# Optimization experiments

Measured on AMD Instinct MI355X. Metric: run time of the kernel, lower is better.

Reference implementation:

```python
import jax, jax.numpy as jnp
import numpy as np

B, T, N_IN, N = 64, 512, 256, 512

def setup_inputs() -> dict:
    key = jax.random.key(0)
    k1, k2, k3 = jax.random.split(key, 3)
    x = jax.random.normal(k1, (B, T, N_IN), dtype=jnp.float32)
    # match nn.Linear default init scale roughly (uniform +-1/sqrt(fan_in))
    W_ih = jax.random.uniform(k2, (N, N_IN), dtype=jnp.float32, minval=-1.0, maxval=1.0) / np.sqrt(N_IN)
    W_hh = jax.random.uniform(k3, (N, N), dtype=jnp.float32, minval=-1.0, maxval=1.0) / np.sqrt(N)
    return {"x": x, "W_ih": W_ih, "W_hh": W_hh}

def reference(x, W_ih, W_hh):
    # h_t = W_hh @ tanh(h_{t-1}) + W_ih @ x_t, h_0 = 0 (pre-activation hidden stored)
    # x: [B, T, n_in] (batch_first). Precompute input projections for all steps.
    xp = jnp.einsum('btc,nc->tbn', x, W_ih)  # [T, B, N]

    def step(h, xp_t):
        h_new = jnp.tanh(h) @ W_hh.T + xp_t  # [B, N]
        return h_new, h_new

    h0 = jnp.zeros((x.shape[0], W_hh.shape[0]), dtype=x.dtype)
    _, hs = jax.lax.scan(step, h0, xp)  # hs: [T, B, N]
    return jnp.swapaxes(hs, 0, 1)  # [B, T, N], batch_first output
```

## Files before the change

kernel.cpp:

```cpp
#include <hip/hip_runtime.h>
#include <hip/hip_bf16.h>
#include <stdint.h>

#define B_   64
#define T_   512
#define NIN_ 256
#define N_   512

typedef _Float16 half2_t __attribute__((ext_vector_type(2)));

#if defined(__has_builtin)
#if __has_builtin(__builtin_amdgcn_fdot2)
#define HAVE_FDOT2 1
#endif
#endif

__device__ __forceinline__ float dot2acc(unsigned int a, unsigned int b, float c) {
#ifdef HAVE_FDOT2
  return __builtin_amdgcn_fdot2(__builtin_bit_cast(half2_t, a),
                                __builtin_bit_cast(half2_t, b), c, false);
#else
  half2_t ha = __builtin_bit_cast(half2_t, a), hb = __builtin_bit_cast(half2_t, b);
  c += (float)ha[0] * (float)hb[0];
  c += (float)ha[1] * (float)hb[1];
  return c;
#endif
}

__device__ __forceinline__ float fast_tanh(float x) {
  float e = __expf(2.0f * x);
  return 1.0f - 2.0f / (e + 1.0f);
}

__global__ __launch_bounds__(256) void xproj(const float* __restrict__ x,
                                             const float* __restrict__ Wih,
                                             float* __restrict__ out) {
  const int tid = threadIdx.x;
  const int bm = blockIdx.x;
  const int bn = blockIdx.y;
  const int tm = tid & 15;
  const int tn = tid >> 4;
  const int m0 = bm << 7;
  const int n0 = bn << 7;

  __shared__ float xt[32][132];
  __shared__ float wt[32][132];

  float acc[8][8];
#pragma unroll
  for (int i = 0; i < 8; ++i) {
#pragma unroll
    for (int j = 0; j < 8; ++j) acc[i][j] = 0.f;
  }

  for (int ko = 0; ko < NIN_; ko += 32) {
#pragma unroll
    for (int it = 0; it < 4; ++it) {
      const int fidx = it * 256 + tid;
      const int mm = fidx >> 3;
      const int k4 = (fidx & 7) << 2;
      const float4 vx = *(const float4*)(x + (size_t)(m0 + mm) * NIN_ + ko + k4);
      xt[k4 + 0][mm] = vx.x; xt[k4 + 1][mm] = vx.y;
      xt[k4 + 2][mm] = vx.z; xt[k4 + 3][mm] = vx.w;
      const float4 vw = *(const float4*)(Wih + (size_t)(n0 + mm) * NIN_ + ko + k4);
      wt[k4 + 0][mm] = vw.x; wt[k4 + 1][mm] = vw.y;
      wt[k4 + 2][mm] = vw.z; wt[k4 + 3][mm] = vw.w;
    }
    __syncthreads();
#pragma unroll 4
    for (int kk = 0; kk < 32; ++kk) {
      float a[8], b[8];
      *(float4*)&a[0] = *(const float4*)&xt[kk][8 * tm];
      *(float4*)&a[4] = *(const float4*)&xt[kk][8 * tm + 4];
      *(float4*)&b[0] = *(const float4*)&wt[kk][8 * tn];
      *(float4*)&b[4] = *(const float4*)&wt[kk][8 * tn + 4];
#pragma unroll
      for (int i = 0; i < 8; ++i) {
#pragma unroll
        for (int j = 0; j < 8; ++j) acc[i][j] = fmaf(a[i], b[j], acc[i][j]);
      }
    }
    __syncthreads();
  }

#pragma unroll
  for (int i = 0; i < 8; ++i) {
    float4 v0 = make_float4(acc[i][0], acc[i][1], acc[i][2], acc[i][3]);
    float4 v1 = make_float4(acc[i][4], acc[i][5], acc[i][6], acc[i][7]);
    float* p = out + (size_t)(m0 + 8 * tm + i) * N_ + n0 + 8 * tn;
    *(float4*)p = v0;
    *((float4*)p + 1) = v1;
  }
}

__global__ __launch_bounds__(512, 1) void rnn_scan(const float* __restrict__ Whh,
                                                   float* __restrict__ out,
                                                   unsigned long long* __restrict__ ex) {
  const int blk = blockIdx.x;
  const int m = blk >> 6;
  const int b = blk & 63;
  const int tid = threadIdx.x;
  const int wv = tid >> 6;
  const int lane = tid & 63;
  const int g = wv >> 2;
  const int q = wv & 3;
  const int nloc = g * 64 + lane;
  const int ng = m * 128 + nloc;

  unsigned int w[64];
  {
    const float* wr = Whh + (size_t)ng * N_ + q * 128;
#pragma unroll
    for (int j = 0; j < 64; ++j) {
      half2_t h;
      h[0] = (_Float16)wr[2 * j];
      h[1] = (_Float16)wr[2 * j + 1];
      w[j] = __builtin_bit_cast(unsigned int, h);
    }
  }

  __shared__ uint4 thp4[64];
  __shared__ float red[8][64];
  __shared__ float thf[128];

  float* outb = out + (size_t)b * T_ * N_;
  unsigned long long* exb = ex + (size_t)b * 2 * 256;

  for (int t = 1; t < T_; ++t) {
    float xp = 0.f;
    if (tid < 128) xp = outb[(size_t)t * N_ + m * 128 + tid];

    if (t == 1) {
      if (tid < 256) {
        float2 h0 = *(const float2*)(outb + 2 * tid);
        half2_t hp;
        hp[0] = (_Float16)fast_tanh(h0.x);
        hp[1] = (_Float16)fast_tanh(h0.y);
        ((unsigned int*)thp4)[tid] = __builtin_bit_cast(unsigned int, hp);
      }
    } else {
      if (tid < 192) {
        const int pr = tid + (tid >= m * 64 ? 64 : 0);
        const int slot = (t - 1) & 1;
        unsigned long long v;
        for (;;) {
          v = __hip_atomic_load(&exb[slot * 256 + pr], __ATOMIC_RELAXED,
                                __HIP_MEMORY_SCOPE_AGENT);
          if ((unsigned int)(v >> 32) == (unsigned int)(t - 1)) break;
          __builtin_amdgcn_s_sleep(1);
        }
        ((unsigned int*)thp4)[pr] = (unsigned int)v;
      }
    }
    __syncthreads();

    float acc = 0.f;
    const uint4* tq = &thp4[q * 16];
#pragma unroll
    for (int j4 = 0; j4 < 16; ++j4) {
      uint4 tv = tq[j4];
      acc = dot2acc(w[4 * j4 + 0], tv.x, acc);
      acc = dot2acc(w[4 * j4 + 1], tv.y, acc);
      acc = dot2acc(w[4 * j4 + 2], tv.z, acc);
      acc = dot2acc(w[4 * j4 + 3], tv.w, acc);
    }
    red[wv][lane] = acc;
    __syncthreads();

    if (tid < 128) {
      const int gg = tid >> 6, ll = tid & 63;
      float y = red[gg * 4 + 0][ll] + red[gg * 4 + 1][ll] +
                red[gg * 4 + 2][ll] + red[gg * 4 + 3][ll] + xp;
      outb[(size_t)t * N_ + m * 128 + tid] = y;
      thf[tid] = fast_tanh(y);
    }
    __syncthreads();

    if (tid < 64) {
      half2_t hp;
      hp[0] = (_Float16)thf[2 * tid];
      hp[1] = (_Float16)thf[2 * tid + 1];
      const unsigned int pk = __builtin_bit_cast(unsigned int, hp);
      ((unsigned int*)thp4)[m * 64 + tid] = pk;
      const int slot = t & 1;
      __hip_atomic_store(&exb[slot * 256 + m * 64 + tid],
                         ((unsigned long long)(unsigned int)t << 32) | pk,
                         __ATOMIC_RELAXED, __HIP_MEMORY_SCOPE_AGENT);
    }
  }
}

extern "C" void kernel_launch(void* const* d_in, const int* in_sizes, int n_in,
                              void* d_out, int out_size, void* d_ws, size_t ws_size,
                              hipStream_t stream) {
  const float* x   = (const float*)d_in[0];
  const float* Wih = (const float*)d_in[1];
  const float* Whh = (const float*)d_in[2];
  float* out = (float*)d_out;
  unsigned long long* ex = (unsigned long long*)d_ws;

  hipMemsetAsync(d_ws, 0, (size_t)B_ * 2 * 256 * 8, stream);

  dim3 g1(256, 4);
  xproj<<<g1, 256, 0, stream>>>(x, Wih, out);
  rnn_scan<<<256, 512, 0, stream>>>(Whh, out, ex);
}
```

Measured before the change: 818.2 us.

## Split scan block into compute and polling warps with double-buffered shared state

Result: slower. 892.1 us (+9.0%).

```diff
diff --git a/kernel.cpp b/kernel.cpp
--- a/kernel.cpp
+++ b/kernel.cpp
@@ -48,10 +48,9 @@
 
   float acc[8][8];
 #pragma unroll
-  for (int i = 0; i < 8; ++i) {
+  for (int i = 0; i < 8; ++i)
 #pragma unroll
     for (int j = 0; j < 8; ++j) acc[i][j] = 0.f;
-  }
 
   for (int ko = 0; ko < NIN_; ko += 32) {
 #pragma unroll
@@ -75,10 +74,9 @@
       *(float4*)&b[0] = *(const float4*)&wt[kk][8 * tn];
       *(float4*)&b[4] = *(const float4*)&wt[kk][8 * tn + 4];
 #pragma unroll
-      for (int i = 0; i < 8; ++i) {
+      for (int i = 0; i < 8; ++i)
 #pragma unroll
         for (int j = 0; j < 8; ++j) acc[i][j] = fmaf(a[i], b[j], acc[i][j]);
-      }
     }
     __syncthreads();
   }
@@ -93,7 +91,7 @@
   }
 }
 
-__global__ __launch_bounds__(512, 1) void rnn_scan(const float* __restrict__ Whh,
+__global__ __launch_bounds__(448, 2) void rnn_scan(const float* __restrict__ Whh,
                                                    float* __restrict__ out,
                                                    unsigned long long* __restrict__ ex) {
   const int blk = blockIdx.x;
@@ -102,90 +100,88 @@
   const int tid = threadIdx.x;
   const int wv = tid >> 6;
   const int lane = tid & 63;
-  const int g = wv >> 2;
-  const int q = wv & 3;
-  const int nloc = g * 64 + lane;
-  const int ng = m * 128 + nloc;
-
-  unsigned int w[64];
-  {
-    const float* wr = Whh + (size_t)ng * N_ + q * 128;
-#pragma unroll
-    for (int j = 0; j < 64; ++j) {
-      half2_t h;
-      h[0] = (_Float16)wr[2 * j];
-      h[1] = (_Float16)wr[2 * j + 1];
-      w[j] = __builtin_bit_cast(unsigned int, h);
-    }
-  }
-
-  __shared__ uint4 thp4[64];
-  __shared__ float red[8][64];
-  __shared__ float thf[128];
+
+  __shared__ __align__(16) unsigned int thp[2][256];
 
   float* outb = out + (size_t)b * T_ * N_;
   unsigned long long* exb = ex + (size_t)b * 2 * 256;
 
-  for (int t = 1; t < T_; ++t) {
-    float xp = 0.f;
-    if (tid < 128) xp = outb[(size_t)t * N_ + m * 128 + tid];
-
-    if (t == 1) {
-      if (tid < 256) {
-        float2 h0 = *(const float2*)(outb + 2 * tid);
+  if (tid < 256) {
+    float2 h0 = *(const float2*)(outb + 2 * tid);
+    half2_t hp;
+    hp[0] = (_Float16)fast_tanh(h0.x);
+    hp[1] = (_Float16)fast_tanh(h0.y);
+    thp[0][tid] = __builtin_bit_cast(unsigned int, hp);
+  }
+
+  if (wv < 4) {
+    const int cl = tid;
+    const int nn = cl >> 1;
+    const int hh = cl & 1;
+    const int gn = m * 128 + nn;
+    const bool even = (hh == 0);
+    const bool q0 = ((cl & 3) == 0);
+    const int pidx = m * 64 + (cl >> 2);
+
+    unsigned int w[128];
+    {
+      const float* wr = Whh + (size_t)gn * N_ + hh * 256;
+#pragma unroll
+      for (int j = 0; j < 128; ++j) {
+        half2_t h;
+        h[0] = (_Float16)wr[2 * j];
+        h[1] = (_Float16)wr[2 * j + 1];
+        w[j] = __builtin_bit_cast(unsigned int, h);
+      }
+    }
+    __syncthreads();
+
+    for (int t = 1; t < T_; ++t) {
+      float xp = 0.f;
+      if (even) xp = outb[(size_t)t * N_ + gn];
+
+      const uint4* tq = (const uint4*)&thp[(t - 1) & 1][hh * 128];
+      float acc = 0.f;
+#pragma unroll
+      for (int j4 = 0; j4 < 32; ++j4) {
+        uint4 tv = tq[j4];
+        acc = dot2acc(w[4 * j4 + 0], tv.x, acc);
+        acc = dot2acc(w[4 * j4 + 1], tv.y, acc);
+        acc = dot2acc(w[4 * j4 + 2], tv.z, acc);
+        acc = dot2acc(w[4 * j4 + 3], tv.w, acc);
+      }
+      float y = acc + __shfl_xor(acc, 1) + xp;
+      float th = 0.f;
+      if (even) th = fast_tanh(y);
+      float thn = __shfl_xor(th, 2);
+      if (q0) {
         half2_t hp;
-        hp[0] = (_Float16)fast_tanh(h0.x);
-        hp[1] = (_Float16)fast_tanh(h0.y);
-        ((unsigned int*)thp4)[tid] = __builtin_bit_cast(unsigned int, hp);
-      }
-    } else {
-      if (tid < 192) {
-        const int pr = tid + (tid >= m * 64 ? 64 : 0);
-        const int slot = (t - 1) & 1;
+        hp[0] = (_Float16)th;
+        hp[1] = (_Float16)thn;
+        const unsigned int pk = __builtin_bit_cast(unsigned int, hp);
+        thp[t & 1][pidx] = pk;
+        __hip_atomic_store(&exb[(t & 1) * 256 + pidx],
+                           ((unsigned long long)(unsigned int)t << 32) | pk,
+                           __ATOMIC_RELAXED, __HIP_MEMORY_SCOPE_AGENT);
+      }
+      if (even) __builtin_nontemporal_store(y, &outb[(size_t)t * N_ + gn]);
+      __syncthreads();
+    }
+  } else {
+    const int s = (wv - 4) * 64 + lane;
+    const int pr = s + (s >= m * 64 ? 64 : 0);
+    __syncthreads();
+
+    for (int t = 1; t < T_; ++t) {
+      if (t < T_ - 1) {
         unsigned long long v;
-        for (;;) {
-          v = __hip_atomic_load(&exb[slot * 256 + pr], __ATOMIC_RELAXED,
+        do {
+          v = __hip_atomic_load(&exb[(t & 1) * 256 + pr], __ATOMIC_RELAXED,
                                 __HIP_MEMORY_SCOPE_AGENT);
-          if ((unsigned int)(v >> 32) == (unsigned int)(t - 1)) break;
-          __builtin_amdgcn_s_sleep(1);
-        }
-        ((unsigned int*)thp4)[pr] = (unsigned int)v;
-      }
-    }
-    __syncthreads();
-
-    float acc = 0.f;
-    const uint4* tq = &thp4[q * 16];
-#pragma unroll
-    for (int j4 = 0; j4 < 16; ++j4) {
-      uint4 tv = tq[j4];
-      acc = dot2acc(w[4 * j4 + 0], tv.x, acc);
-      acc = dot2acc(w[4 * j4 + 1], tv.y, acc);
-      acc = dot2acc(w[4 * j4 + 2], tv.z, acc);
-      acc = dot2acc(w[4 * j4 + 3], tv.w, acc);
-    }
-    red[wv][lane] = acc;
-    __syncthreads();
-
-    if (tid < 128) {
-      const int gg = tid >> 6, ll = tid & 63;
-      float y = red[gg * 4 + 0][ll] + red[gg * 4 + 1][ll] +
-                red[gg * 4 + 2][ll] + red[gg * 4 + 3][ll] + xp;
-      outb[(size_t)t * N_ + m * 128 + tid] = y;
-      thf[tid] = fast_tanh(y);
-    }
-    __syncthreads();
-
-    if (tid < 64) {
-      half2_t hp;
-      hp[0] = (_Float16)thf[2 * tid];
-      hp[1] = (_Float16)thf[2 * tid + 1];
-      const unsigned int pk = __builtin_bit_cast(unsigned int, hp);
-      ((unsigned int*)thp4)[m * 64 + tid] = pk;
-      const int slot = t & 1;
-      __hip_atomic_store(&exb[slot * 256 + m * 64 + tid],
-                         ((unsigned long long)(unsigned int)t << 32) | pk,
-                         __ATOMIC_RELAXED, __HIP_MEMORY_SCOPE_AGENT);
+        } while ((unsigned int)(v >> 32) != (unsigned int)t);
+        thp[t & 1][pr] = (unsigned int)v;
+      }
+      __syncthreads();
     }
   }
 }
@@ -203,5 +199,5 @@
 
   dim3 g1(256, 4);
   xproj<<<g1, 256, 0, stream>>>(x, Wih, out);
-  rnn_scan<<<256, 512, 0, stream>>>(Whh, out, ex);
-}
+  rnn_scan<<<256, 448, 0, stream>>>(Whh, out, ex);
+}
```
